# Performance work log

Hardware: AMD Instinct MI355X
Metric: run time of the kernel (lower is better)

The kernel has to match this reference:

```python
import jax, jax.numpy as jnp
import numpy as np

QMAX = 127.0  # 8-bit symmetric: levels in [-128, 127]


def _ste_round(v):
    # round with straight-through estimator (matches torch fake-quant training)
    return v + jax.lax.stop_gradient(jnp.round(v) - v)


def _act_fake_quant(x, clip_factor):
    # per-tensor symmetric fake quant with learnable clip (lac):
    # clip range = sigmoid(clip_factor) * max|x|
    scale = jax.nn.sigmoid(clip_factor) * jnp.max(jnp.abs(x)) / QMAX
    return jnp.clip(_ste_round(x / scale), -QMAX - 1.0, QMAX) * scale


def _weight_fake_quant(w):
    # per-output-channel symmetric fake quant; w: [out, in]
    scale = jnp.max(jnp.abs(w), axis=1, keepdims=True) / QMAX
    return jnp.clip(_ste_round(w / scale), -QMAX - 1.0, QMAX) * scale


def setup_inputs() -> dict:
    key = jax.random.key(0)
    k1, k2, k3, k4 = jax.random.split(key, 4)
    B, S, H, I = 8, 8192, 1024, 2816
    return {
        "x": jax.random.normal(k1, (B, S, H), dtype=jnp.float32),
        "clip_x": jnp.full((1,), 4.0, dtype=jnp.float32),     # sigmoid(4) ~ 0.982
        "clip_down": jnp.full((1,), 4.0, dtype=jnp.float32),
        "w_gate": jax.random.normal(k2, (I, H), dtype=jnp.float32) * 0.02,
        "w_up": jax.random.normal(k3, (I, H), dtype=jnp.float32) * 0.02,
        "w_down": jax.random.normal(k4, (H, I), dtype=jnp.float32) * 0.02,
    }


def reference(x, clip_x, clip_down, w_gate, w_up, w_down):
    # _trans_forward: quantize act -> gate/up quant-matmul -> SwiGLU -> quantize -> down quant-matmul
    xq = _act_fake_quant(x, clip_x[0])                       # [B,S,H]
    gate = jnp.einsum("bsh,ih->bsi", xq, _weight_fake_quant(w_gate))
    up = jnp.einsum("bsh,ih->bsi", xq, _weight_fake_quant(w_up))
    h = _act_fake_quant(jax.nn.silu(gate) * up, clip_down[0])  # [B,S,I]
    return jnp.einsum("bsi,hi->bsh", h, _weight_fake_quant(w_down))
```

## Files before the change

### kernel.cpp

```cpp
#include <hip/hip_runtime.h>
#include <stdint.h>

typedef __attribute__((ext_vector_type(4))) int i32x4;

typedef const __attribute__((address_space(1))) void gvoid_t;
typedef __attribute__((address_space(3))) void lvoid_t;

#define GLD16(g, l) __builtin_amdgcn_global_load_lds((gvoid_t*)(g), (lvoid_t*)(l), 16, 0, 0)
#define FENCE() asm volatile("" ::: "memory")
#define BARRIER() do { FENCE(); __builtin_amdgcn_s_barrier(); FENCE(); } while (0)
#define VMCNT4() asm volatile("s_waitcnt vmcnt(4)" ::: "memory")
#define VMCNT0() asm volatile("s_waitcnt vmcnt(0)" ::: "memory")

__device__ inline int q1mul(float x, float r) {
    return (int)fminf(fmaxf(rintf(x * r), -128.f), 127.f);
}
__device__ inline int q1div(float x, float s) {
    return (int)fminf(fmaxf(rintf(x / s), -128.f), 127.f);
}
__device__ inline int pack4(float4 v, float r) {
    return (q1mul(v.x, r) & 255) | ((q1mul(v.y, r) & 255) << 8) |
           ((q1mul(v.z, r) & 255) << 16) | ((q1mul(v.w, r) & 255) << 24);
}

__global__ void k_absmax(const float* __restrict__ x, size_t n4, unsigned int* __restrict__ out) {
    size_t S = (size_t)gridDim.x * blockDim.x;
    size_t i = (size_t)blockIdx.x * blockDim.x + threadIdx.x;
    const float4* x4 = (const float4*)x;
    float m0 = 0.f, m1 = 0.f, m2 = 0.f, m3 = 0.f;
    for (; i + 3 * S < n4; i += 4 * S) {
        float4 v0 = x4[i], v1 = x4[i + S], v2 = x4[i + 2 * S], v3 = x4[i + 3 * S];
        m0 = fmaxf(m0, fmaxf(fmaxf(fabsf(v0.x), fabsf(v0.y)), fmaxf(fabsf(v0.z), fabsf(v0.w))));
        m1 = fmaxf(m1, fmaxf(fmaxf(fabsf(v1.x), fabsf(v1.y)), fmaxf(fabsf(v1.z), fabsf(v1.w))));
        m2 = fmaxf(m2, fmaxf(fmaxf(fabsf(v2.x), fabsf(v2.y)), fmaxf(fabsf(v2.z), fabsf(v2.w))));
        m3 = fmaxf(m3, fmaxf(fmaxf(fabsf(v3.x), fabsf(v3.y)), fmaxf(fabsf(v3.z), fabsf(v3.w))));
    }
    for (; i < n4; i += S) {
        float4 v = x4[i];
        m0 = fmaxf(m0, fmaxf(fmaxf(fabsf(v.x), fabsf(v.y)), fmaxf(fabsf(v.z), fabsf(v.w))));
    }
    float m = fmaxf(fmaxf(m0, m1), fmaxf(m2, m3));
    #pragma unroll
    for (int off = 32; off > 0; off >>= 1) m = fmaxf(m, __shfl_xor(m, off, 64));
    if ((threadIdx.x & 63) == 0) atomicMax(out, __float_as_uint(m));
}

__global__ void k_scale(const float* __restrict__ clip, const unsigned int* __restrict__ maxbits,
                        float* __restrict__ s_out) {
    float m = __uint_as_float(*maxbits);
    float sig = 1.f / (1.f + expf(-clip[0]));
    float s = sig * m / 127.f;
    s_out[0] = s;
    s_out[1] = 1.f / s;
}

__global__ void k_quant_f32_i8(const float* __restrict__ in, int4* __restrict__ out,
                               const float* __restrict__ sptr, size_t n16) {
    float r = sptr[1];
    size_t S = (size_t)gridDim.x * blockDim.x;
    size_t i = (size_t)blockIdx.x * blockDim.x + threadIdx.x;
    const float4* in4 = (const float4*)in;
    for (; i < n16; i += S) {
        float4 v0 = in4[4 * i], v1 = in4[4 * i + 1], v2 = in4[4 * i + 2], v3 = in4[4 * i + 3];
        int4 o;
        o.x = pack4(v0, r); o.y = pack4(v1, r); o.z = pack4(v2, r); o.w = pack4(v3, r);
        out[i] = o;
    }
}

__global__ void k_quant_h16_i8(const short* __restrict__ h16, const float* __restrict__ sblk,
                               const float* __restrict__ sh, int4* __restrict__ qh, size_t nchunks) {
    const float rh = sh[1] * (1.f / 32766.f);
    size_t S = (size_t)gridDim.x * blockDim.x;
    size_t i = (size_t)blockIdx.x * blockDim.x + threadIdx.x;
    for (; i < nchunks; i += S) {
        int row = (int)(i / 176);
        int col = (int)(i - (size_t)row * 176) * 16;
        float f = sblk[(row >> 8) * 22 + (col >> 7)] * rh;
        const int4* p = (const int4*)(h16 + (size_t)row * 2816 + col);
        int4 lo = p[0], hi = p[1];
        int w[8] = {lo.x, lo.y, lo.z, lo.w, hi.x, hi.y, hi.z, hi.w};
        int ob[4];
        #pragma unroll
        for (int j = 0; j < 4; ++j) {
            int q0 = q1mul((float)(short)(w[2 * j] & 0xFFFF), f);
            int q1 = q1mul((float)(short)(w[2 * j] >> 16), f);
            int q2 = q1mul((float)(short)(w[2 * j + 1] & 0xFFFF), f);
            int q3 = q1mul((float)(short)(w[2 * j + 1] >> 16), f);
            ob[j] = (q0 & 255) | ((q1 & 255) << 8) | ((q2 & 255) << 16) | ((q3 & 255) << 24);
        }
        int4 o; o.x = ob[0]; o.y = ob[1]; o.z = ob[2]; o.w = ob[3];
        qh[i] = o;
    }
}

__global__ void k_quant_w_i8(const float* __restrict__ W, int8_t* __restrict__ Q,
                             float* __restrict__ srow, int cols) {
    int row = blockIdx.x;
    const float* w = W + (size_t)row * cols;
    float m = 0.f;
    for (int c = threadIdx.x; c < cols; c += 256) m = fmaxf(m, fabsf(w[c]));
    #pragma unroll
    for (int off = 32; off > 0; off >>= 1) m = fmaxf(m, __shfl_xor(m, off, 64));
    __shared__ float red[4];
    if ((threadIdx.x & 63) == 0) red[threadIdx.x >> 6] = m;
    __syncthreads();
    if (threadIdx.x == 0) {
        float mm = fmaxf(fmaxf(red[0], red[1]), fmaxf(red[2], red[3]));
        red[0] = mm / 127.f;
        srow[row] = mm / 127.f;
    }
    __syncthreads();
    float s = red[0];
    for (int c = threadIdx.x; c < cols; c += 256)
        Q[(size_t)row * cols + c] = (int8_t)q1div(w[c], s);
}

__global__ __launch_bounds__(512, 2) void k_gemm1_i8(
    const int8_t* __restrict__ Aq, const int8_t* __restrict__ Bg, const int8_t* __restrict__ Bu,
    const float* __restrict__ sg, const float* __restrict__ su, const float* __restrict__ sx,
    short* __restrict__ H16, float* __restrict__ sblk, unsigned int* __restrict__ maxh,
    int nt_base)
{
    constexpr int K = 1024, N = 2816, NT = K / 128, BUF = 65536;
    __shared__ int8_t lds[2 * BUF];

    const int wgl = (int)blockIdx.x >> 3;
    const int xcd = (int)blockIdx.x & 7;
    const int mtspan = (int)(gridDim.x >> 3) / 11;
    const int mt = xcd * mtspan + wgl / 11;
    const int nt = nt_base + wgl % 11;
    const int m0 = mt * 256, n0 = nt * 128;
    const int tid = threadIdx.x;
    const int wid = tid >> 6, lane = tid & 63;
    const int wm = wid >> 2, wn = wid & 3;
    const int lr = lane & 15, lk = lane >> 4;

    const int srow = tid >> 2;
    const int scol = ((tid & 3) ^ ((srow >> 1) & 3)) << 4;
    const int8_t* gA0 = Aq + (size_t)(m0 + srow) * K + scol;
    const int8_t* gA1 = gA0 + (size_t)128 * K;
    const int8_t* gG  = Bg + (size_t)(n0 + srow) * K + scol;
    const int8_t* gU  = Bu + (size_t)(n0 + srow) * K + scol;
    const int ldst = wid << 10;

    const int swz = (lk ^ ((lr >> 1) & 3)) << 4;

    i32x4 accg[8][2] = {};
    i32x4 accu[8][2] = {};

    {
        int8_t* Lw = &lds[0];
        GLD16(gA0,      Lw + ldst);         GLD16(gA1,      Lw + 8192  + ldst);
        GLD16(gG,       Lw + 32768 + ldst); GLD16(gU,       Lw + 40960 + ldst);
        GLD16(gA0 + 64, Lw + 16384 + ldst); GLD16(gA1 + 64, Lw + 24576 + ldst);
        GLD16(gG  + 64, Lw + 49152 + ldst); GLD16(gU  + 64, Lw + 57344 + ldst);
    }
    VMCNT4();
    BARRIER();

    for (int t = 0; t < NT; ++t) {
        const bool st = (t + 1 < NT);
        const size_t kk = (size_t)(t + 1) * 128;
        const int8_t* Lr = &lds[(t & 1) * BUF];
        int8_t* Lw = &lds[((t + 1) & 1) * BUF];
        i32x4 a[4], bg[2], bu[2];

        #pragma unroll
        for (int mi = 0; mi < 4; ++mi)
            a[mi] = *(const i32x4*)(Lr + (wm * 128 + mi * 16 + lr) * 64 + swz);
        #pragma unroll
        for (int ni = 0; ni < 2; ++ni) {
            bg[ni] = *(const i32x4*)(Lr + 32768 + (wn * 32 + ni * 16 + lr) * 64 + swz);
            bu[ni] = *(const i32x4*)(Lr + 40960 + (wn * 32 + ni * 16 + lr) * 64 + swz);
        }
        if (st) { GLD16(gA0 + kk, Lw + ldst); GLD16(gA1 + kk, Lw + 8192 + ldst); }
        BARRIER();
        __builtin_amdgcn_s_setprio(1);
        #pragma unroll
        for (int mi = 0; mi < 4; ++mi)
            #pragma unroll
            for (int ni = 0; ni < 2; ++ni) {
                accg[mi][ni] = __builtin_amdgcn_mfma_i32_16x16x64_i8(a[mi], bg[ni], accg[mi][ni], 0, 0, 0);
                accu[mi][ni] = __builtin_amdgcn_mfma_i32_16x16x64_i8(a[mi], bu[ni], accu[mi][ni], 0, 0, 0);
            }
        __builtin_amdgcn_s_setprio(0);
        BARRIER();

        #pragma unroll
        for (int mi = 0; mi < 4; ++mi)
            a[mi] = *(const i32x4*)(Lr + (wm * 128 + 64 + mi * 16 + lr) * 64 + swz);
        if (st) { GLD16(gG + kk, Lw + 32768 + ldst); GLD16(gU + kk, Lw + 40960 + ldst); }
        BARRIER();
        __builtin_amdgcn_s_setprio(1);
        #pragma unroll
        for (int mi = 0; mi < 4; ++mi)
            #pragma unroll
            for (int ni = 0; ni < 2; ++ni) {
                accg[4 + mi][ni] = __builtin_amdgcn_mfma_i32_16x16x64_i8(a[mi], bg[ni], accg[4 + mi][ni], 0, 0, 0);
                accu[4 + mi][ni] = __builtin_amdgcn_mfma_i32_16x16x64_i8(a[mi], bu[ni], accu[4 + mi][ni], 0, 0, 0);
            }
        __builtin_amdgcn_s_setprio(0);
        if (st) { VMCNT4(); } else { VMCNT0(); }
        BARRIER();

        #pragma unroll
        for (int mi = 0; mi < 4; ++mi)
            a[mi] = *(const i32x4*)(Lr + 16384 + (wm * 128 + mi * 16 + lr) * 64 + swz);
        #pragma unroll
        for (int ni = 0; ni < 2; ++ni) {
            bg[ni] = *(const i32x4*)(Lr + 49152 + (wn * 32 + ni * 16 + lr) * 64 + swz);
            bu[ni] = *(const i32x4*)(Lr + 57344 + (wn * 32 + ni * 16 + lr) * 64 + swz);
        }
        if (st) { GLD16(gA0 + kk + 64, Lw + 16384 + ldst); GLD16(gA1 + kk + 64, Lw + 24576 + ldst); }
        BARRIER();
        __builtin_amdgcn_s_setprio(1);
        #pragma unroll
        for (int mi = 0; mi < 4; ++mi)
            #pragma unroll
            for (int ni = 0; ni < 2; ++ni) {
                accg[mi][ni] = __builtin_amdgcn_mfma_i32_16x16x64_i8(a[mi], bg[ni], accg[mi][ni], 0, 0, 0);
                accu[mi][ni] = __builtin_amdgcn_mfma_i32_16x16x64_i8(a[mi], bu[ni], accu[mi][ni], 0, 0, 0);
            }
        __builtin_amdgcn_s_setprio(0);
        BARRIER();

        #pragma unroll
        for (int mi = 0; mi < 4; ++mi)
            a[mi] = *(const i32x4*)(Lr + 16384 + (wm * 128 + 64 + mi * 16 + lr) * 64 + swz);
        if (st) { GLD16(gG + kk + 64, Lw + 49152 + ldst); GLD16(gU + kk + 64, Lw + 57344 + ldst); }
        BARRIER();
        __builtin_amdgcn_s_setprio(1);
        #pragma unroll
        for (int mi = 0; mi < 4; ++mi)
            #pragma unroll
            for (int ni = 0; ni < 2; ++ni) {
                accg[4 + mi][ni] = __builtin_amdgcn_mfma_i32_16x16x64_i8(a[mi], bg[ni], accg[4 + mi][ni], 0, 0, 0);
                accu[4 + mi][ni] = __builtin_amdgcn_mfma_i32_16x16x64_i8(a[mi], bu[ni], accu[4 + mi][ni], 0, 0, 0);
            }
        __builtin_amdgcn_s_setprio(0);
        if (st) { VMCNT4(); }
        BARRIER();
    }

    const float s_x = sx[0];
    float lmax = 0.f;
    #pragma unroll
    for (int ni = 0; ni < 2; ++ni) {
        const int nl = wn * 32 + ni * 16 + lr;
        const float fg = s_x * sg[n0 + nl];
        const float fu = s_x * su[n0 + nl];
        #pragma unroll
        for (int mi = 0; mi < 8; ++mi) {
            const int rowb = wm * 128 + mi * 16 + lk * 4;
            #pragma unroll
            for (int r = 0; r < 4; ++r) {
                float g = (float)accg[mi][ni][r] * fg;
                float u = (float)accu[mi][ni][r] * fu;
                float h = g * u / (1.f + expf(-g));
                *(float*)(lds + ((rowb + r) << 9) + (nl << 2)) = h;
                lmax = fmaxf(lmax, fabsf(h));
            }
        }
    }
    #pragma unroll
    for (int off = 32; off > 0; off >>= 1) lmax = fmaxf(lmax, __shfl_xor(lmax, off, 64));
    unsigned int* slot = (unsigned int*)&sblk[mt * 22 + nt];
    if (lane == 0) atomicMax(slot, __float_as_uint(lmax));
    BARRIER();
    const float bmax = __uint_as_float(*slot);
    if (tid == 0) atomicMax(maxh, __float_as_uint(bmax));
    const float qs = 32766.f / fmaxf(bmax, 1e-20f);
    uint* H16u = (uint*)H16;
    #pragma unroll
    for (int k = 0; k < 32; ++k) {
        const int fidx = 2 * (tid + k * 512);
        const int row = fidx >> 7, col = fidx & 127;
        const float2 hv = *(const float2*)(lds + (fidx << 2));
        const int s0 = (int)rintf(hv.x * qs), s1 = (int)rintf(hv.y * qs);
        H16u[((size_t)(m0 + row) * N + n0 + col) >> 1] = (s0 & 0xFFFF) | (s1 << 16);
    }
}

__global__ __launch_bounds__(512, 2) void k_gemm2_i8(
    const int8_t* __restrict__ Aq, const int8_t* __restrict__ Bw,
    const float* __restrict__ sw, const float* __restrict__ sh,
    float* __restrict__ Out)
{
    constexpr int K = 2816, N = 1024, NT = K / 128, BUF = 65536;
    __shared__ int8_t lds[2 * BUF];

    const int chunk = gridDim.x >> 3;
    const int wg = ((int)blockIdx.x & 7) * chunk + ((int)blockIdx.x >> 3);
    const int mt = wg >> 2, nt = wg & 3;
    const int m0 = mt * 256, n0 = nt * 256;
    const int tid = threadIdx.x;
    const int wid = tid >> 6, lane = tid & 63;
    const int wm = wid >> 2, wn = wid & 3;
    const int lr = lane & 15, lk = lane >> 4;

    const int srow = tid >> 2;
    const int scol = ((tid & 3) ^ ((srow >> 1) & 3)) << 4;
    const int8_t* gA0 = Aq + (size_t)(m0 + srow) * K + scol;
    const int8_t* gA1 = gA0 + (size_t)128 * K;
    const int8_t* gB0 = Bw + (size_t)(n0 + srow) * K + scol;
    const int8_t* gB1 = gB0 + (size_t)128 * K;
    const int ldst = wid << 10;

    const int swz = (lk ^ ((lr >> 1) & 3)) << 4;

    i32x4 acc[8][4] = {};

    {
        int8_t* Lw = &lds[0];
        GLD16(gA0,      Lw + ldst);         GLD16(gA1,      Lw + 8192  + ldst);
        GLD16(gB0,      Lw + 32768 + ldst); GLD16(gB1,      Lw + 40960 + ldst);
        GLD16(gA0 + 64, Lw + 16384 + ldst); GLD16(gA1 + 64, Lw + 24576 + ldst);
        GLD16(gB0 + 64, Lw + 49152 + ldst); GLD16(gB1 + 64, Lw + 57344 + ldst);
    }
    VMCNT4();
    BARRIER();

    for (int t = 0; t < NT; ++t) {
        const bool st = (t + 1 < NT);
        const size_t kk = (size_t)(t + 1) * 128;
        const int8_t* Lr = &lds[(t & 1) * BUF];
        int8_t* Lw = &lds[((t + 1) & 1) * BUF];
        i32x4 a[4], b[4];

        #pragma unroll
        for (int mi = 0; mi < 4; ++mi)
            a[mi] = *(const i32x4*)(Lr + (wm * 128 + mi * 16 + lr) * 64 + swz);
        #pragma unroll
        for (int ni = 0; ni < 4; ++ni)
            b[ni] = *(const i32x4*)(Lr + 32768 + (wn * 64 + ni * 16 + lr) * 64 + swz);
        if (st) { GLD16(gA0 + kk, Lw + ldst); GLD16(gA1 + kk, Lw + 8192 + ldst); }
        BARRIER();
        __builtin_amdgcn_s_setprio(1);
        #pragma unroll
        for (int mi = 0; mi < 4; ++mi)
            #pragma unroll
            for (int ni = 0; ni < 4; ++ni)
                acc[mi][ni] = __builtin_amdgcn_mfma_i32_16x16x64_i8(a[mi], b[ni], acc[mi][ni], 0, 0, 0);
        __builtin_amdgcn_s_setprio(0);
        BARRIER();

        #pragma unroll
        for (int mi = 0; mi < 4; ++mi)
            a[mi] = *(const i32x4*)(Lr + (wm * 128 + 64 + mi * 16 + lr) * 64 + swz);
        if (st) { GLD16(gB0 + kk, Lw + 32768 + ldst); GLD16(gB1 + kk, Lw + 40960 + ldst); }
        BARRIER();
        __builtin_amdgcn_s_setprio(1);
        #pragma unroll
        for (int mi = 0; mi < 4; ++mi)
            #pragma unroll
            for (int ni = 0; ni < 4; ++ni)
                acc[4 + mi][ni] = __builtin_amdgcn_mfma_i32_16x16x64_i8(a[mi], b[ni], acc[4 + mi][ni], 0, 0, 0);
        __builtin_amdgcn_s_setprio(0);
        if (st) { VMCNT4(); } else { VMCNT0(); }
        BARRIER();

        #pragma unroll
        for (int mi = 0; mi < 4; ++mi)
            a[mi] = *(const i32x4*)(Lr + 16384 + (wm * 128 + mi * 16 + lr) * 64 + swz);
        #pragma unroll
        for (int ni = 0; ni < 4; ++ni)
            b[ni] = *(const i32x4*)(Lr + 49152 + (wn * 64 + ni * 16 + lr) * 64 + swz);
        if (st) { GLD16(gA0 + kk + 64, Lw + 16384 + ldst); GLD16(gA1 + kk + 64, Lw + 24576 + ldst); }
        BARRIER();
        __builtin_amdgcn_s_setprio(1);
        #pragma unroll
        for (int mi = 0; mi < 4; ++mi)
            #pragma unroll
            for (int ni = 0; ni < 4; ++ni)
                acc[mi][ni] = __builtin_amdgcn_mfma_i32_16x16x64_i8(a[mi], b[ni], acc[mi][ni], 0, 0, 0);
        __builtin_amdgcn_s_setprio(0);
        BARRIER();

        #pragma unroll
        for (int mi = 0; mi < 4; ++mi)
            a[mi] = *(const i32x4*)(Lr + 16384 + (wm * 128 + 64 + mi * 16 + lr) * 64 + swz);
        if (st) { GLD16(gB0 + kk + 64, Lw + 49152 + ldst); GLD16(gB1 + kk + 64, Lw + 57344 + ldst); }
        BARRIER();
        __builtin_amdgcn_s_setprio(1);
        #pragma unroll
        for (int mi = 0; mi < 4; ++mi)
            #pragma unroll
            for (int ni = 0; ni < 4; ++ni)
                acc[4 + mi][ni] = __builtin_amdgcn_mfma_i32_16x16x64_i8(a[mi], b[ni], acc[4 + mi][ni], 0, 0, 0);
        __builtin_amdgcn_s_setprio(0);
        if (st) { VMCNT4(); }
        BARRIER();
    }

    const float s_h = sh[0];
    #pragma unroll
    for (int ni = 0; ni < 4; ++ni) {
        const int n = n0 + wn * 64 + ni * 16 + lr;
        const float f = s_h * sw[n];
        #pragma unroll
        for (int mi = 0; mi < 8; ++mi) {
            const int mb = m0 + wm * 128 + mi * 16 + lk * 4;
            #pragma unroll
            for (int r = 0; r < 4; ++r)
                Out[(size_t)(mb + r) * N + n] = (float)acc[mi][ni][r] * f;
        }
    }
}

extern "C" void kernel_launch(void* const* d_in, const int* in_sizes, int n_in,
                              void* d_out, int out_size, void* d_ws, size_t ws_size,
                              hipStream_t stream) {
    const float* x       = (const float*)d_in[0];
    const float* clip_x  = (const float*)d_in[1];
    const float* clip_dn = (const float*)d_in[2];
    const float* w_gate  = (const float*)d_in[3];
    const float* w_up    = (const float*)d_in[4];
    const float* w_down  = (const float*)d_in[5];
    float* out = (float*)d_out;

    const int Hd = 1024, Id = 2816;
    const int M = in_sizes[0] / Hd;
    const size_t nx = (size_t)M * Hd;
    const size_t nh = (size_t)M * Id;

    char* ws = (char*)d_ws;
    size_t off = 0;
    auto alloc = [&](size_t bytes) -> char* {
        char* p = ws + off;
        off = (off + bytes + 255) & ~(size_t)255;
        return p;
    };
    unsigned int* max_slots = (unsigned int*)alloc(8);
    float* sxp = (float*)alloc(8);
    float* shp = (float*)alloc(8);
    int8_t* qx  = (int8_t*)alloc(nx);
    int8_t* qwg = (int8_t*)alloc((size_t)Id * Hd);
    int8_t* qwu = (int8_t*)alloc((size_t)Id * Hd);
    int8_t* qwd = (int8_t*)alloc((size_t)Hd * Id);
    float* swg = (float*)alloc((size_t)Id * 4);
    float* swu = (float*)alloc((size_t)Id * 4);
    float* swd = (float*)alloc((size_t)Hd * 4);
    int8_t* qh = (int8_t*)alloc(nh);
    short* h16 = (short*)alloc(nh * 2);
    const size_t sblk_bytes = (size_t)(M / 256) * 22 * 4;
    float* sblk = (float*)alloc(sblk_bytes);

    hipMemsetAsync(max_slots, 0, 8, stream);
    hipMemsetAsync(sblk, 0, sblk_bytes, stream);

    k_absmax<<<4096, 256, 0, stream>>>(x, nx / 4, &max_slots[0]);
    k_scale<<<1, 1, 0, stream>>>(clip_x, &max_slots[0], sxp);
    k_quant_f32_i8<<<2048, 256, 0, stream>>>(x, (int4*)qx, sxp, nx / 16);
    k_quant_w_i8<<<Id, 256, 0, stream>>>(w_gate, qwg, swg, Hd);
    k_quant_w_i8<<<Id, 256, 0, stream>>>(w_up, qwu, swu, Hd);
    k_quant_w_i8<<<Hd, 256, 0, stream>>>(w_down, qwd, swd, Id);

    const int g1grid = (M / 256) * 11;
    k_gemm1_i8<<<g1grid, 512, 0, stream>>>(qx, qwg, qwu, swg, swu, sxp, h16, sblk, &max_slots[1], 0);
    k_gemm1_i8<<<g1grid, 512, 0, stream>>>(qx, qwg, qwu, swg, swu, sxp, h16, sblk, &max_slots[1], 11);
    k_scale<<<1, 1, 0, stream>>>(clip_dn, &max_slots[1], shp);
    k_quant_h16_i8<<<4096, 256, 0, stream>>>(h16, sblk, shp, (int4*)qh, nh / 16);

    k_gemm2_i8<<<(M / 256) * (Hd / 256), 512, 0, stream>>>(qh, qwd, swd, shp, out);
}
```

Before: 1.156 ms.

## Double-buffer register fragments and cut barriers in int8 GEMM main loops

Both int8 GEMM kernels get a restructured K loop. LDS fragments are kept in two register sets (A/B ping-pong), so the next sub-tile's LDS reads are issued before the current MFMA block, and the first fragments of the next tile are prefetched from the write buffer. Eight barriers per iteration become two combined vmcnt+barrier gates, and sched_barrier fences stop the compiler from reordering loads across MFMA groups. In exchange, register pressure rises and the hazard reasoning gets subtle: global loads into the write buffer now overlap with reads that are guarded by fewer barriers.

```diff
diff --git a/kernel.cpp b/kernel.cpp
--- a/kernel.cpp
+++ b/kernel.cpp
@@ -9,8 +9,8 @@
 #define GLD16(g, l) __builtin_amdgcn_global_load_lds((gvoid_t*)(g), (lvoid_t*)(l), 16, 0, 0)
 #define FENCE() asm volatile("" ::: "memory")
 #define BARRIER() do { FENCE(); __builtin_amdgcn_s_barrier(); FENCE(); } while (0)
-#define VMCNT4() asm volatile("s_waitcnt vmcnt(4)" ::: "memory")
-#define VMCNT0() asm volatile("s_waitcnt vmcnt(0)" ::: "memory")
+#define SCHEDB() __builtin_amdgcn_sched_barrier(0)
+#define GATE(n) asm volatile("s_waitcnt vmcnt(" #n ")\n\ts_barrier" ::: "memory")
 
 __device__ inline int q1mul(float x, float r) {
     return (int)fminf(fmaxf(rintf(x * r), -128.f), 127.f);
@@ -116,6 +116,16 @@
         Q[(size_t)row * cols + c] = (int8_t)q1div(w[c], s);
 }
 
+#define MFMA_G1(AF, BG, BU, OFF)                                                              \
+    _Pragma("unroll")                                                                         \
+    for (int mi = 0; mi < 4; ++mi) {                                                          \
+        _Pragma("unroll")                                                                     \
+        for (int ni = 0; ni < 2; ++ni) {                                                      \
+            accg[(OFF) + mi][ni] = __builtin_amdgcn_mfma_i32_16x16x64_i8(AF[mi], BG[ni], accg[(OFF) + mi][ni], 0, 0, 0); \
+            accu[(OFF) + mi][ni] = __builtin_amdgcn_mfma_i32_16x16x64_i8(AF[mi], BU[ni], accu[(OFF) + mi][ni], 0, 0, 0); \
+        }                                                                                     \
+    }
+
 __global__ __launch_bounds__(512, 2) void k_gemm1_i8(
     const int8_t* __restrict__ Aq, const int8_t* __restrict__ Bg, const int8_t* __restrict__ Bu,
     const float* __restrict__ sg, const float* __restrict__ su, const float* __restrict__ sx,
@@ -145,9 +155,13 @@
     const int ldst = wid << 10;
 
     const int swz = (lk ^ ((lr >> 1) & 3)) << 4;
+    const int aoff = (wm * 128 + lr) * 64 + swz;
+    const int boffG = 32768 + (wn * 32 + lr) * 64 + swz;
+    const int boffU = 40960 + (wn * 32 + lr) * 64 + swz;
 
     i32x4 accg[8][2] = {};
     i32x4 accu[8][2] = {};
+    i32x4 aA[4], aB[4], bgA[2], buA[2], bgB[2], buB[2];
 
     {
         int8_t* Lw = &lds[0];
@@ -156,92 +170,71 @@
         GLD16(gA0 + 64, Lw + 16384 + ldst); GLD16(gA1 + 64, Lw + 24576 + ldst);
         GLD16(gG  + 64, Lw + 49152 + ldst); GLD16(gU  + 64, Lw + 57344 + ldst);
     }
-    VMCNT4();
-    BARRIER();
+    GATE(4);
+    {
+        const int8_t* Lr = &lds[0];
+        #pragma unroll
+        for (int mi = 0; mi < 4; ++mi) aA[mi] = *(const i32x4*)(Lr + aoff + mi * 1024);
+        #pragma unroll
+        for (int ni = 0; ni < 2; ++ni) {
+            bgA[ni] = *(const i32x4*)(Lr + boffG + ni * 1024);
+            buA[ni] = *(const i32x4*)(Lr + boffU + ni * 1024);
+        }
+    }
 
     for (int t = 0; t < NT; ++t) {
         const bool st = (t + 1 < NT);
-        const size_t kk = (size_t)(t + 1) * 128;
         const int8_t* Lr = &lds[(t & 1) * BUF];
         int8_t* Lw = &lds[((t + 1) & 1) * BUF];
-        i32x4 a[4], bg[2], bu[2];
-
-        #pragma unroll
-        for (int mi = 0; mi < 4; ++mi)
-            a[mi] = *(const i32x4*)(Lr + (wm * 128 + mi * 16 + lr) * 64 + swz);
+        const size_t kk = (size_t)(t + 1) * 128;
+
+        #pragma unroll
+        for (int mi = 0; mi < 4; ++mi) aB[mi] = *(const i32x4*)(Lr + aoff + 4096 + mi * 1024);
+        if (st) { GLD16(gA0 + kk, Lw + ldst); GLD16(gA1 + kk, Lw + 8192 + ldst); }
+        SCHEDB();
+        __builtin_amdgcn_s_setprio(1);
+        MFMA_G1(aA, bgA, buA, 0);
+        __builtin_amdgcn_s_setprio(0);
+        if (st) { GATE(2); } else { GATE(0); }
+
+        #pragma unroll
+        for (int mi = 0; mi < 4; ++mi) aA[mi] = *(const i32x4*)(Lr + 16384 + aoff + mi * 1024);
         #pragma unroll
         for (int ni = 0; ni < 2; ++ni) {
-            bg[ni] = *(const i32x4*)(Lr + 32768 + (wn * 32 + ni * 16 + lr) * 64 + swz);
-            bu[ni] = *(const i32x4*)(Lr + 40960 + (wn * 32 + ni * 16 + lr) * 64 + swz);
-        }
-        if (st) { GLD16(gA0 + kk, Lw + ldst); GLD16(gA1 + kk, Lw + 8192 + ldst); }
-        BARRIER();
-        __builtin_amdgcn_s_setprio(1);
-        #pragma unroll
-        for (int mi = 0; mi < 4; ++mi)
+            bgB[ni] = *(const i32x4*)(Lr + 16384 + boffG + ni * 1024);
+            buB[ni] = *(const i32x4*)(Lr + 16384 + boffU + ni * 1024);
+        }
+        if (st) { GLD16(gG + kk, Lw + 32768 + ldst); GLD16(gU + kk, Lw + 40960 + ldst); }
+        SCHEDB();
+        __builtin_amdgcn_s_setprio(1);
+        MFMA_G1(aB, bgA, buA, 4);
+        __builtin_amdgcn_s_setprio(0);
+
+        #pragma unroll
+        for (int mi = 0; mi < 4; ++mi) aB[mi] = *(const i32x4*)(Lr + 16384 + aoff + 4096 + mi * 1024);
+        if (st) { GLD16(gA0 + kk + 64, Lw + 16384 + ldst); GLD16(gA1 + kk + 64, Lw + 24576 + ldst);
+                  GLD16(gG + kk + 64, Lw + 49152 + ldst);  GLD16(gU + kk + 64, Lw + 57344 + ldst); }
+        SCHEDB();
+        __builtin_amdgcn_s_setprio(1);
+        MFMA_G1(aA, bgB, buB, 0);
+        __builtin_amdgcn_s_setprio(0);
+        if (st) { GATE(4); } else { GATE(0); }
+
+        if (st) {
+            #pragma unroll
+            for (int mi = 0; mi < 4; ++mi) aA[mi] = *(const i32x4*)(Lw + aoff + mi * 1024);
             #pragma unroll
             for (int ni = 0; ni < 2; ++ni) {
-                accg[mi][ni] = __builtin_amdgcn_mfma_i32_16x16x64_i8(a[mi], bg[ni], accg[mi][ni], 0, 0, 0);
-                accu[mi][ni] = __builtin_amdgcn_mfma_i32_16x16x64_i8(a[mi], bu[ni], accu[mi][ni], 0, 0, 0);
+                bgA[ni] = *(const i32x4*)(Lw + boffG + ni * 1024);
+                buA[ni] = *(const i32x4*)(Lw + boffU + ni * 1024);
             }
-        __builtin_amdgcn_s_setprio(0);
-        BARRIER();
-
-        #pragma unroll
-        for (int mi = 0; mi < 4; ++mi)
-            a[mi] = *(const i32x4*)(Lr + (wm * 128 + 64 + mi * 16 + lr) * 64 + swz);
-        if (st) { GLD16(gG + kk, Lw + 32768 + ldst); GLD16(gU + kk, Lw + 40960 + ldst); }
-        BARRIER();
-        __builtin_amdgcn_s_setprio(1);
-        #pragma unroll
-        for (int mi = 0; mi < 4; ++mi)
-            #pragma unroll
-            for (int ni = 0; ni < 2; ++ni) {
-                accg[4 + mi][ni] = __builtin_amdgcn_mfma_i32_16x16x64_i8(a[mi], bg[ni], accg[4 + mi][ni], 0, 0, 0);
-                accu[4 + mi][ni] = __builtin_amdgcn_mfma_i32_16x16x64_i8(a[mi], bu[ni], accu[4 + mi][ni], 0, 0, 0);
-            }
-        __builtin_amdgcn_s_setprio(0);
-        if (st) { VMCNT4(); } else { VMCNT0(); }
-        BARRIER();
-
-        #pragma unroll
-        for (int mi = 0; mi < 4; ++mi)
-            a[mi] = *(const i32x4*)(Lr + 16384 + (wm * 128 + mi * 16 + lr) * 64 + swz);
-        #pragma unroll
-        for (int ni = 0; ni < 2; ++ni) {
-            bg[ni] = *(const i32x4*)(Lr + 49152 + (wn * 32 + ni * 16 + lr) * 64 + swz);
-            bu[ni] = *(const i32x4*)(Lr + 57344 + (wn * 32 + ni * 16 + lr) * 64 + swz);
-        }
-        if (st) { GLD16(gA0 + kk + 64, Lw + 16384 + ldst); GLD16(gA1 + kk + 64, Lw + 24576 + ldst); }
-        BARRIER();
-        __builtin_amdgcn_s_setprio(1);
-        #pragma unroll
-        for (int mi = 0; mi < 4; ++mi)
-            #pragma unroll
-            for (int ni = 0; ni < 2; ++ni) {
-                accg[mi][ni] = __builtin_amdgcn_mfma_i32_16x16x64_i8(a[mi], bg[ni], accg[mi][ni], 0, 0, 0);
-                accu[mi][ni] = __builtin_amdgcn_mfma_i32_16x16x64_i8(a[mi], bu[ni], accu[mi][ni], 0, 0, 0);
-            }
-        __builtin_amdgcn_s_setprio(0);
-        BARRIER();
-
-        #pragma unroll
-        for (int mi = 0; mi < 4; ++mi)
-            a[mi] = *(const i32x4*)(Lr + 16384 + (wm * 128 + 64 + mi * 16 + lr) * 64 + swz);
-        if (st) { GLD16(gG + kk + 64, Lw + 49152 + ldst); GLD16(gU + kk + 64, Lw + 57344 + ldst); }
-        BARRIER();
-        __builtin_amdgcn_s_setprio(1);
-        #pragma unroll
-        for (int mi = 0; mi < 4; ++mi)
-            #pragma unroll
-            for (int ni = 0; ni < 2; ++ni) {
-                accg[4 + mi][ni] = __builtin_amdgcn_mfma_i32_16x16x64_i8(a[mi], bg[ni], accg[4 + mi][ni], 0, 0, 0);
-                accu[4 + mi][ni] = __builtin_amdgcn_mfma_i32_16x16x64_i8(a[mi], bu[ni], accu[4 + mi][ni], 0, 0, 0);
-            }
-        __builtin_amdgcn_s_setprio(0);
-        if (st) { VMCNT4(); }
-        BARRIER();
-    }
+        }
+        SCHEDB();
+        __builtin_amdgcn_s_setprio(1);
+        MFMA_G1(aB, bgB, buB, 4);
+        __builtin_amdgcn_s_setprio(0);
+    }
+    BARRIER();
 
     const float s_x = sx[0];
     float lmax = 0.f;
@@ -282,6 +275,14 @@
     }
 }
 
+#define MFMA_G2(AF, BF, OFF)                                                                  \
+    _Pragma("unroll")                                                                         \
+    for (int mi = 0; mi < 4; ++mi) {                                                          \
+        _Pragma("unroll")                                                                     \
+        for (int ni = 0; ni < 4; ++ni)                                                        \
+            acc[(OFF) + mi][ni] = __builtin_amdgcn_mfma_i32_16x16x64_i8(AF[mi], BF[ni], acc[(OFF) + mi][ni], 0, 0, 0); \
+    }
+
 __global__ __launch_bounds__(512, 2) void k_gemm2_i8(
     const int8_t* __restrict__ Aq, const int8_t* __restrict__ Bw,
     const float* __restrict__ sw, const float* __restrict__ sh,
@@ -308,8 +309,11 @@
     const int ldst = wid << 10;
 
     const int swz = (lk ^ ((lr >> 1) & 3)) << 4;
+    const int aoff = (wm * 128 + lr) * 64 + swz;
+    const int boff = 32768 + (wn * 64 + lr) * 64 + swz;
 
     i32x4 acc[8][4] = {};
+    i32x4 aA[4], aB[4], bA[4], bB[4];
 
     {
         int8_t* Lw = &lds[0];
@@ -318,79 +322,60 @@
         GLD16(gA0 + 64, Lw + 16384 + ldst); GLD16(gA1 + 64, Lw + 24576 + ldst);
         GLD16(gB0 + 64, Lw + 49152 + ldst); GLD16(gB1 + 64, Lw + 57344 + ldst);
     }
-    VMCNT4();
-    BARRIER();
+    GATE(4);
+    {
+        const int8_t* Lr = &lds[0];
+        #pragma unroll
+        for (int mi = 0; mi < 4; ++mi) aA[mi] = *(const i32x4*)(Lr + aoff + mi * 1024);
+        #pragma unroll
+        for (int ni = 0; ni < 4; ++ni) bA[ni] = *(const i32x4*)(Lr + boff + ni * 1024);
+    }
 
     for (int t = 0; t < NT; ++t) {
         const bool st = (t + 1 < NT);
-        const size_t kk = (size_t)(t + 1) * 128;
         const int8_t* Lr = &lds[(t & 1) * BUF];
         int8_t* Lw = &lds[((t + 1) & 1) * BUF];
-        i32x4 a[4], b[4];
-
-        #pragma unroll
-        for (int mi = 0; mi < 4; ++mi)
-            a[mi] = *(const i32x4*)(Lr + (wm * 128 + mi * 16 + lr) * 64 + swz);
-        #pragma unroll
-        for (int ni = 0; ni < 4; ++ni)
-            b[ni] = *(const i32x4*)(Lr + 32768 + (wn * 64 + ni * 16 + lr) * 64 + swz);
+        const size_t kk = (size_t)(t + 1) * 128;
+
+        #pragma unroll
+        for (int mi = 0; mi < 4; ++mi) aB[mi] = *(const i32x4*)(Lr + aoff + 4096 + mi * 1024);
         if (st) { GLD16(gA0 + kk, Lw + ldst); GLD16(gA1 + kk, Lw + 8192 + ldst); }
-        BARRIER();
-        __builtin_amdgcn_s_setprio(1);
-        #pragma unroll
-        for (int mi = 0; mi < 4; ++mi)
-            #pragma unroll
-            for (int ni = 0; ni < 4; ++ni)
-                acc[mi][ni] = __builtin_amdgcn_mfma_i32_16x16x64_i8(a[mi], b[ni], acc[mi][ni], 0, 0, 0);
-        __builtin_amdgcn_s_setprio(0);
-        BARRIER();
-
-        #pragma unroll
-        for (int mi = 0; mi < 4; ++mi)
-            a[mi] = *(const i32x4*)(Lr + (wm * 128 + 64 + mi * 16 + lr) * 64 + swz);
+        SCHEDB();
+        __builtin_amdgcn_s_setprio(1);
+        MFMA_G2(aA, bA, 0);
+        __builtin_amdgcn_s_setprio(0);
+        if (st) { GATE(2); } else { GATE(0); }
+
+        #pragma unroll
+        for (int mi = 0; mi < 4; ++mi) aA[mi] = *(const i32x4*)(Lr + 16384 + aoff + mi * 1024);
+        #pragma unroll
+        for (int ni = 0; ni < 4; ++ni) bB[ni] = *(const i32x4*)(Lr + 16384 + boff + ni * 1024);
         if (st) { GLD16(gB0 + kk, Lw + 32768 + ldst); GLD16(gB1 + kk, Lw + 40960 + ldst); }
-        BARRIER();
-        __builtin_amdgcn_s_setprio(1);
-        #pragma unroll
-        for (int mi = 0; mi < 4; ++mi)
-            #pragma unroll
-            for (int ni = 0; ni < 4; ++ni)
-                acc[4 + mi][ni] = __builtin_amdgcn_mfma_i32_16x16x64_i8(a[mi], b[ni], acc[4 + mi][ni], 0, 0, 0);
-        __builtin_amdgcn_s_setprio(0);
-        if (st) { VMCNT4(); } else { VMCNT0(); }
-        BARRIER();
-
-        #pragma unroll
-        for (int mi = 0; mi < 4; ++mi)
-            a[mi] = *(const i32x4*)(Lr + 16384 + (wm * 128 + mi * 16 + lr) * 64 + swz);
-        #pragma unroll
-        for (int ni = 0; ni < 4; ++ni)
-            b[ni] = *(const i32x4*)(Lr + 49152 + (wn * 64 + ni * 16 + lr) * 64 + swz);
-        if (st) { GLD16(gA0 + kk + 64, Lw + 16384 + ldst); GLD16(gA1 + kk + 64, Lw + 24576 + ldst); }
-        BARRIER();
-        __builtin_amdgcn_s_setprio(1);
-        #pragma unroll
-        for (int mi = 0; mi < 4; ++mi)
-            #pragma unroll
-            for (int ni = 0; ni < 4; ++ni)
-                acc[mi][ni] = __builtin_amdgcn_mfma_i32_16x16x64_i8(a[mi], b[ni], acc[mi][ni], 0, 0, 0);
-        __builtin_amdgcn_s_setprio(0);
-        BARRIER();
-
-        #pragma unroll
-        for (int mi = 0; mi < 4; ++mi)
-            a[mi] = *(const i32x4*)(Lr + 16384 + (wm * 128 + 64 + mi * 16 + lr) * 64 + swz);
-        if (st) { GLD16(gB0 + kk + 64, Lw + 49152 + ldst); GLD16(gB1 + kk + 64, Lw + 57344 + ldst); }
-        BARRIER();
-        __builtin_amdgcn_s_setprio(1);
-        #pragma unroll
-        for (int mi = 0; mi < 4; ++mi)
-            #pragma unroll
-            for (int ni = 0; ni < 4; ++ni)
-                acc[4 + mi][ni] = __builtin_amdgcn_mfma_i32_16x16x64_i8(a[mi], b[ni], acc[4 + mi][ni], 0, 0, 0);
-        __builtin_amdgcn_s_setprio(0);
-        if (st) { VMCNT4(); }
-        BARRIER();
+        SCHEDB();
+        __builtin_amdgcn_s_setprio(1);
+        MFMA_G2(aB, bA, 4);
+        __builtin_amdgcn_s_setprio(0);
+
+        #pragma unroll
+        for (int mi = 0; mi < 4; ++mi) aB[mi] = *(const i32x4*)(Lr + 16384 + aoff + 4096 + mi * 1024);
+        if (st) { GLD16(gA0 + kk + 64, Lw + 16384 + ldst); GLD16(gA1 + kk + 64, Lw + 24576 + ldst);
+                  GLD16(gB0 + kk + 64, Lw + 49152 + ldst); GLD16(gB1 + kk + 64, Lw + 57344 + ldst); }
+        SCHEDB();
+        __builtin_amdgcn_s_setprio(1);
+        MFMA_G2(aA, bB, 0);
+        __builtin_amdgcn_s_setprio(0);
+        if (st) { GATE(4); } else { GATE(0); }
+
+        if (st) {
+            #pragma unroll
+            for (int mi = 0; mi < 4; ++mi) aA[mi] = *(const i32x4*)(Lw + aoff + mi * 1024);
+            #pragma unroll
+            for (int ni = 0; ni < 4; ++ni) bA[ni] = *(const i32x4*)(Lw + boff + ni * 1024);
+        }
+        SCHEDB();
+        __builtin_amdgcn_s_setprio(1);
+        MFMA_G2(aB, bB, 4);
+        __builtin_amdgcn_s_setprio(0);
     }
 
     const float s_h = sh[0];
```

After: 1.137 ms (median of 2 runs). Within noise of the previous version (-1.7%).
